# Performance work log

Measured on AMD Instinct MI355X. Metric: run time of the kernel, lower is better.

## Reference

```python
import jax, jax.numpy as jnp
import numpy as np

B, T_IN, T_OUT = 32, 256, 512
N_MEL, E = 80, 512
A_RNN, D_RNN, PRENET, A_DIM = 1024, 1024, 256, 128
N_FILT, KSIZE = 32, 31


def setup_inputs() -> dict:
    key = jax.random.key(0)
    ks = jax.random.split(key, 20)
    def w(k, shape):
        fan_in = shape[-1] if len(shape) == 2 else shape[1] * shape[2]
        return jax.random.normal(k, shape, jnp.float32) / np.sqrt(fan_in)
    return dict(
        memory=jax.random.normal(ks[0], (B, T_IN, E), jnp.float32),
        decoder_inputs=jax.random.normal(ks[1], (B, N_MEL, T_OUT), jnp.float32),
        memory_lengths=jax.random.randint(ks[2], (B,), T_IN // 2, T_IN + 1).astype(jnp.int32),
        prenet_w1=w(ks[3], (PRENET, N_MEL)),
        prenet_w2=w(ks[4], (PRENET, PRENET)),
        att_rnn_wih=w(ks[5], (4 * A_RNN, PRENET + E)),
        att_rnn_whh=w(ks[6], (4 * A_RNN, A_RNN)),
        att_rnn_b=jnp.zeros((4 * A_RNN,), jnp.float32),
        wq=w(ks[7], (A_DIM, A_RNN)),
        wm=w(ks[8], (A_DIM, E)),
        v=w(ks[9], (1, A_DIM)),
        loc_conv=w(ks[10], (N_FILT, 2, KSIZE)),
        loc_dense=w(ks[11], (A_DIM, N_FILT)),
        dec_rnn_wih=w(ks[12], (4 * D_RNN, A_RNN + E)),
        dec_rnn_whh=w(ks[13], (4 * D_RNN, D_RNN)),
        dec_rnn_b=jnp.zeros((4 * D_RNN,), jnp.float32),
        proj_w=w(ks[14], (N_MEL, D_RNN + E)),
        proj_b=jnp.zeros((N_MEL,), jnp.float32),
        gate_w=w(ks[15], (1, D_RNN + E)),
        gate_b=jnp.zeros((1,), jnp.float32),
    )


def _lstm_cell(x, h, c, wih, whh, b):
    g = x @ wih.T + h @ whh.T + b
    i, f, gg, o = jnp.split(g, 4, axis=-1)
    c2 = jax.nn.sigmoid(f) * c + jax.nn.sigmoid(i) * jnp.tanh(gg)
    h2 = jax.nn.sigmoid(o) * jnp.tanh(c2)
    return h2, c2


def reference(memory, decoder_inputs, memory_lengths, prenet_w1, prenet_w2,
              att_rnn_wih, att_rnn_whh, att_rnn_b, wq, wm, v, loc_conv, loc_dense,
              dec_rnn_wih, dec_rnn_whh, dec_rnn_b, proj_w, proj_b, gate_w, gate_b):
    Bc, Tin, Ec = memory.shape
    # True where padded (masked out of attention)
    pad_mask = jnp.arange(Tin)[None, :] >= memory_lengths[:, None]
    processed_memory = memory @ wm.T  # (B, T_in, A_DIM)

    # parse decoder inputs: (B, n_mel, T_out) -> (T_out, B, n_mel); prepend go frame
    dec_seq = jnp.transpose(decoder_inputs, (2, 0, 1))
    go = jnp.zeros((1, Bc, N_MEL), dec_seq.dtype)
    dec_seq = jnp.concatenate([go, dec_seq], axis=0)[:-1]  # teacher-forced inputs
    # prenet (eval; stochastic dropout removed for determinism)
    x = jax.nn.relu(dec_seq @ prenet_w1.T)
    x = jax.nn.relu(x @ prenet_w2.T)  # (T_out, B, PRENET)

    NEG = jnp.asarray(-1e9, memory.dtype)
    pad = KSIZE // 2

    def step(carry, xt):
        ah, ac, dh, dc, aw, awc, ctx = carry
        # attention RNN
        ah, ac = _lstm_cell(jnp.concatenate([xt, ctx], -1), ah, ac,
                            att_rnn_wih, att_rnn_whh, att_rnn_b)
        # location-sensitive attention
        cat = jnp.stack([aw, awc], axis=1)  # (B, 2, T_in)
        loc = jax.lax.conv_general_dilated(cat, loc_conv, (1,), [(pad, pad)],
                                           dimension_numbers=('NCH', 'OIH', 'NCH'))
        loc = jnp.transpose(loc, (0, 2, 1)) @ loc_dense.T  # (B, T_in, A_DIM)
        pq = ah @ wq.T  # (B, A_DIM)
        e = jnp.tanh(pq[:, None, :] + loc + processed_memory) @ v[0]  # (B, T_in)
        e = jnp.where(pad_mask, NEG, e)
        wgt = jax.nn.softmax(e, axis=1)
        ctx = jnp.einsum('bt,bte->be', wgt, memory)
        awc = awc + wgt
        # decoder RNN
        dh, dc = _lstm_cell(jnp.concatenate([ah, ctx], -1), dh, dc,
                            dec_rnn_wih, dec_rnn_whh, dec_rnn_b)
        pi = jnp.concatenate([dh, ctx], -1)
        mel = pi @ proj_w.T + proj_b
        gate = (pi @ gate_w.T + gate_b)[:, 0]
        return (ah, ac, dh, dc, wgt, awc, ctx), (mel, gate, wgt)

    z = lambda *s: jnp.zeros(s, memory.dtype)
    carry0 = (z(Bc, A_RNN), z(Bc, A_RNN), z(Bc, D_RNN), z(Bc, D_RNN),
              z(Bc, Tin), z(Bc, Tin), z(Bc, Ec))
    _, (mels, gates, aligns) = jax.lax.scan(step, carry0, x)
    mel_out = jnp.transpose(mels, (1, 2, 0))      # (B, n_mel, T_out)
    gate_out = gates.T                             # (B, T_out)
    align_out = jnp.transpose(aligns, (1, 0, 2))   # (B, T_out, T_in)
    return mel_out, gate_out, align_out
```

## Files before the change

### kernel.cpp

```cpp
#include <hip/hip_runtime.h>
#include <hip/hip_bf16.h>
#include <math.h>

typedef __attribute__((ext_vector_type(8))) short bf16x8;
typedef __attribute__((ext_vector_type(4))) float f32x4;

#define B_X2    0u
#define B_PM    8388608u
#define B_WSA   12582912u
#define B_WSD   27262976u
#define B_AHB0  48234496u
#define B_AHB1  48300032u
#define B_DHB0  48365568u
#define B_DHB1  48431104u
#define B_CTXB  48496640u
#define B_AC    48529408u
#define B_DC    48660480u
#define B_AWC   48791552u
#define B_ZERO_START 48234496u
#define B_ZERO_BYTES 589824u
#define B_AHF   48824320u
#define B_DHF0  48955392u
#define B_CTXF0 49086464u
#define B_CTXF1 49152000u
#define B_DHF1  49217536u
#define B_LPM   49348608u
#define B_WQT   53542912u

#define OUT_MEL   0u
#define OUT_GATE  1310720u
#define OUT_ALIGN 1327104u

#define QSM_BYTES 23040

__device__ __forceinline__ float sigf(float x) { return 1.f / (1.f + expf(-x)); }
__device__ __forceinline__ float ftanh(float x) {
    float t = exp2f(x * 2.885390081777927f);
    return 1.f - 2.f * __builtin_amdgcn_rcpf(t + 1.f);
}

#define HOLD(s, b0, b1) (((s) & 1) ? (b0) : (b1))

__global__ __launch_bounds__(256) void prenet_kernel(
    const float* __restrict__ dec_in,
    const float* __restrict__ w1,
    const float* __restrict__ w2,
    __hip_bfloat16* __restrict__ x2)
{
    int b  = blockIdx.x & 31;
    int t0 = (blockIdx.x >> 5) * 16;
    __shared__ float xin[16][80];
    __shared__ float h1[16][257];

    for (int i = threadIdx.x; i < 16 * 80; i += 256) {
        int tt = i / 80, m = i - tt * 80;
        int t = t0 + tt;
        xin[tt][m] = (t == 0) ? 0.f
                   : dec_in[(size_t)b * 80 * 512 + (size_t)m * 512 + (t - 1)];
    }
    __syncthreads();
    for (int i = threadIdx.x; i < 16 * 256; i += 256) {
        int tt = i >> 8, p = i & 255;
        const float* wr = w1 + p * 80;
        float s = 0.f;
        for (int m = 0; m < 80; ++m) s += xin[tt][m] * wr[m];
        h1[tt][p] = fmaxf(s, 0.f);
    }
    __syncthreads();
    for (int i = threadIdx.x; i < 16 * 256; i += 256) {
        int tt = i >> 8, q = i & 255;
        const float* wr = w2 + q * 256;
        float s = 0.f;
        for (int p = 0; p < 256; ++p) s += h1[tt][p] * wr[p];
        int t = t0 + tt;
        x2[(size_t)t * (32 * 256) + b * 256 + q] = __float2bfloat16(fmaxf(s, 0.f));
    }
}

__global__ __launch_bounds__(128) void pm_kernel(
    const float* __restrict__ memory,
    const float* __restrict__ wm,
    float* __restrict__ pm)
{
    int b = blockIdx.y, tt0 = blockIdx.x * 16;
    __shared__ float ms[16][513];
    for (int i = threadIdx.x; i < 16 * 512; i += 128) {
        int tt = i >> 9, e = i & 511;
        ms[tt][e] = memory[(size_t)b * 131072 + (size_t)(tt0 + tt) * 512 + e];
    }
    __syncthreads();
    int d = threadIdx.x;
    float acc[16];
#pragma unroll
    for (int i = 0; i < 16; ++i) acc[i] = 0.f;
    const float* wr = wm + d * 512;
    for (int e = 0; e < 512; ++e) {
        float w = wr[e];
#pragma unroll
        for (int ttl = 0; ttl < 16; ++ttl) acc[ttl] += w * ms[ttl][e];
    }
    for (int ttl = 0; ttl < 16; ++ttl)
        pm[(size_t)b * 32768 + (size_t)(tt0 + ttl) * 128 + d] = acc[ttl];
}

__global__ __launch_bounds__(256) void swizzle_kernel(
    const float* __restrict__ wih, int Kih,
    const float* __restrict__ whh, int Khh,
    __hip_bfloat16* __restrict__ out, int K)
{
    int idx = blockIdx.x * 256 + threadIdx.x;
    int lane = idx & 63;
    int tk = idx >> 6;
    int KB = K >> 5;
    int nt = tk / KB, kb = tk - nt * KB;
    int c = lane & 15;
    int n = (c >> 2) * 1024 + nt * 4 + (c & 3);
    int k = kb * 32 + ((lane >> 4) << 3);
    const float* src; int kk;
    if (k < Kih) { src = wih + (size_t)n * Kih; kk = k; }
    else         { src = whh + (size_t)n * Khh; kk = k - Kih; }
    __hip_bfloat16* op = out + (size_t)idx * 8;
#pragma unroll
    for (int j = 0; j < 8; ++j) op[j] = __float2bfloat16(src[kk + j]);
}

__global__ __launch_bounds__(256) void wqt_kernel(
    const float* __restrict__ wq,
    float* __restrict__ wqT)
{
    int idx = blockIdx.x * 256 + threadIdx.x;
    int k = idx >> 7, d = idx & 127;
    wqT[idx] = wq[(size_t)d * 1024 + k];
}

template<int K, int S0, int S1, int S0STR, int S1STR, int S2STR>
__device__ __forceinline__ void lstm_tile(
    char* smem, int nt,
    const __hip_bfloat16* __restrict__ seg0,
    const __hip_bfloat16* __restrict__ seg1,
    const __hip_bfloat16* __restrict__ seg2,
    const __hip_bfloat16* __restrict__ wsw,
    const float* __restrict__ bias,
    float* __restrict__ c_state,
    float* __restrict__ h_f32,
    __hip_bfloat16* __restrict__ h_bf16)
{
    constexpr int KB  = K / 32;
    constexpr int NCH = K / 256;

    float (*red)[2][4][64] = (float(*)[2][4][64])smem;
    float (*gsum)[17]      = (float(*)[17])(smem + 16384);

    int tid  = threadIdx.x;
    int lane = tid & 63;
    int w    = tid >> 6;
    int r0   = lane & 15;
    int kq   = (lane >> 4) << 3;

    const __hip_bfloat16* wp = wsw + (((size_t)nt * KB + (size_t)w * NCH) * 64 + lane) * 8;
    f32x4 acc0 = {0.f, 0.f, 0.f, 0.f};
    f32x4 acc1 = {0.f, 0.f, 0.f, 0.f};
    int k0 = w * (K / 8);

#pragma unroll
    for (int i = 0; i < NCH; ++i) {
        int kc = k0 + i * 32;
        const __hip_bfloat16* sp; int sstr, off;
        if (kc < S0)           { sp = seg0; sstr = S0STR; off = kc; }
        else if (kc < S0 + S1) { sp = seg1; sstr = S1STR; off = kc - S0; }
        else                   { sp = seg2; sstr = S2STR; off = kc - S0 - S1; }
        int ko = off + kq;
        bf16x8 a0 = *(const bf16x8*)(sp + (size_t)r0 * sstr + ko);
        bf16x8 a1 = *(const bf16x8*)(sp + (size_t)(r0 + 16) * sstr + ko);
        bf16x8 bb = *(const bf16x8*)(wp + (size_t)i * 512);
        acc0 = __builtin_amdgcn_mfma_f32_16x16x32_bf16(a0, bb, acc0, 0, 0, 0);
        acc1 = __builtin_amdgcn_mfma_f32_16x16x32_bf16(a1, bb, acc1, 0, 0, 0);
    }

#pragma unroll
    for (int r = 0; r < 4; ++r) {
        red[w][0][r][lane] = acc0[r];
        red[w][1][r][lane] = acc1[r];
    }
    __syncthreads();

    {
        int b = tid >> 4, c = tid & 15;
        int mt = b >> 4, bm = b & 15;
        int lidx = ((bm >> 2) << 4) + c, rg = bm & 3;
        float s = 0.f;
#pragma unroll
        for (int ks = 0; ks < 8; ++ks) s += red[ks][mt][rg][lidx];
        gsum[b][c] = s;
    }
    __syncthreads();

    if (tid < 128) {
        int b = tid & 31, jl = tid >> 5;
        int j = nt * 4 + jl;
        float gi = gsum[b][jl]      + bias[j];
        float gf = gsum[b][4 + jl]  + bias[1024 + j];
        float gg = gsum[b][8 + jl]  + bias[2048 + j];
        float go = gsum[b][12 + jl] + bias[3072 + j];
        float cv = c_state[b * 1024 + j];
        float c2 = sigf(gf) * cv + sigf(gi) * tanhf(gg);
        float h2 = sigf(go) * tanhf(c2);
        c_state[b * 1024 + j] = c2;
        h_f32[b * 1024 + j]   = h2;
        h_bf16[b * 1024 + j]  = __float2bfloat16(h2);
    }
}

__global__ __launch_bounds__(512, 2) void qstep_kernel(
    const __hip_bfloat16* __restrict__ x2b,
    __hip_bfloat16* __restrict__ ctxb,
    __hip_bfloat16* __restrict__ ahb0, __hip_bfloat16* __restrict__ ahb1,
    __hip_bfloat16* __restrict__ dhb0, __hip_bfloat16* __restrict__ dhb1,
    const __hip_bfloat16* __restrict__ wswA,
    const __hip_bfloat16* __restrict__ wswD,
    const float* __restrict__ a_b, const float* __restrict__ d_b,
    float* __restrict__ ac, float* __restrict__ dc,
    float* __restrict__ ahf,
    float* __restrict__ dhf0, float* __restrict__ dhf1,
    const float* __restrict__ ctxf0, const float* __restrict__ ctxf1,
    const float* __restrict__ proj_w, const float* __restrict__ proj_b,
    const float* __restrict__ gate_w, const float* __restrict__ gate_b,
    float* __restrict__ out_mel, float* __restrict__ out_gate,
    const float* __restrict__ lconv, const float* __restrict__ ldense,
    const float* __restrict__ pm,
    const float* __restrict__ awc, const float* __restrict__ align_out,
    float* __restrict__ lpmbuf,
    int t)
{
    __shared__ char smem[QSM_BYTES];
    int blk = blockIdx.x;
    int tid = threadIdx.x;

    if (blk < 256) {
        if (t < 0) return;
        lstm_tile<2560, 1024, 512, 1024, 512, 1024>(
            smem, blk,
            HOLD(t, ahb0, ahb1), ctxb, HOLD(t - 1, dhb0, dhb1),
            wswD, d_b, dc,
            HOLD(t, dhf1, dhf0), HOLD(t, dhb0, dhb1));
        return;
    }

    if (blk < 512) {
        int s = t + 1;
        if (s > 511) return;
        lstm_tile<1792, 256, 512, 256, 512, 1024>(
            smem, blk - 256,
            x2b + (size_t)s * 8192, ctxb, HOLD(s - 1, ahb0, ahb1),
            wswA, a_b, ac, ahf, HOLD(s, ahb0, ahb1));
        return;
    }

    if (blk < 544) {
        if (t + 1 > 511) return;
        int b = blk - 512;
        __hip_bfloat16 (*locb)[40] = (__hip_bfloat16(*)[40])smem;
        float* aw_s  = (float*)(smem + 20480);
        float* awc_s = (float*)(smem + 21632);

        if (tid < 288) {
            int tt = tid - 15;
            float a = 0.f, c = 0.f;
            if (tt >= 0 && tt < 256) {
                a = (t >= 0) ? align_out[(size_t)b * 131072 + (size_t)t * 256 + tt] : 0.f;
                c = awc[b * 256 + tt];
            }
            aw_s[tid] = a; awc_s[tid] = c;
        }
        __syncthreads();

        for (int it = 0; it < 2; ++it) {
            int item = tid + it * 512;
            int f = item >> 5, ttg = item & 31;
            const float* kcA = lconv + f * 62;
            const float* kcB = kcA + 31;
            float ka[31], kb_[31];
#pragma unroll
            for (int k = 0; k < 31; ++k) { ka[k] = kcA[k]; kb_[k] = kcB[k]; }
            float acc[8];
#pragma unroll
            for (int s = 0; s < 8; ++s) acc[s] = 0.f;
            int base = ttg * 8;
#pragma unroll
            for (int u = 0; u < 38; ++u) {
                float av = aw_s[base + u];
                float cv = awc_s[base + u];
#pragma unroll
                for (int s = 0; s < 8; ++s) {
                    int k = u - s;
                    if (k >= 0 && k < 31) {
                        acc[s] = fmaf(ka[k], av, acc[s]);
                        acc[s] = fmaf(kb_[k], cv, acc[s]);
                    }
                }
            }
#pragma unroll
            for (int s = 0; s < 8; ++s)
                locb[base + s][f] = __float2bfloat16(acc[s]);
        }
        __syncthreads();

        {
            int lane = tid & 63;
            int w    = tid >> 6;
            int c    = lane & 15, q = lane >> 4;

            bf16x8 Bf[8];
#pragma unroll
            for (int tc = 0; tc < 8; ++tc) {
                int d = tc * 16 + c;
                const float* lp = ldense + d * 32 + q * 8;
                float4 f0 = *(const float4*)lp;
                float4 f1 = *(const float4*)(lp + 4);
                union { bf16x8 vv; __hip_bfloat16 h[8]; } u;
                u.h[0] = __float2bfloat16(f0.x); u.h[1] = __float2bfloat16(f0.y);
                u.h[2] = __float2bfloat16(f0.z); u.h[3] = __float2bfloat16(f0.w);
                u.h[4] = __float2bfloat16(f1.x); u.h[5] = __float2bfloat16(f1.y);
                u.h[6] = __float2bfloat16(f1.z); u.h[7] = __float2bfloat16(f1.w);
                Bf[tc] = u.vv;
            }
#pragma unroll
            for (int half = 0; half < 2; ++half) {
                int mt = w * 2 + half;
                bf16x8 Af = *(const bf16x8*)&locb[mt * 16 + c][q * 8];
                f32x4 zero = {0.f, 0.f, 0.f, 0.f};
#pragma unroll
                for (int tc = 0; tc < 8; ++tc) {
                    f32x4 P = __builtin_amdgcn_mfma_f32_16x16x32_bf16(Af, Bf[tc], zero, 0, 0, 0);
                    int d = tc * 16 + c;
#pragma unroll
                    for (int r = 0; r < 4; ++r) {
                        int ttp = mt * 16 + q * 4 + r;
                        size_t ix = ((size_t)b << 15) + (size_t)ttp * 128 + d;
                        lpmbuf[ix] = P[r] + pm[ix];
                    }
                }
            }
        }
        return;
    }

    {
        if (t < 1) return;
        int pb = blk - 544;
        int b = pb >> 1, half = pb & 1;
        int tp = t - 1;
        const float* dh = HOLD(tp, dhf1, dhf0);
        const float* cx = HOLD(tp, ctxf1, ctxf0);
        float* pi = (float*)smem;
        for (int i = tid; i < 1024; i += 512) pi[i] = dh[b * 1024 + i];
        if (tid < 512) pi[1024 + tid] = cx[b * 512 + tid];
        __syncthreads();
        int w = tid >> 6, lane = tid & 63;
        int nOut = half ? 41 : 40;
        for (int o = w; o < nOut; o += 8) {
            bool isGate = (half && o == 40);
            int m = half * 40 + o;
            const float* wr = isGate ? gate_w : (proj_w + (size_t)m * 1536);
            float s = 0.f;
#pragma unroll
            for (int c = 0; c < 6; ++c) {
                float4 wv = *(const float4*)(wr + c * 256 + lane * 4);
                const float* pp = pi + c * 256 + lane * 4;
                s += wv.x * pp[0] + wv.y * pp[1] + wv.z * pp[2] + wv.w * pp[3];
            }
#pragma unroll
            for (int mm = 32; mm >= 1; mm >>= 1) s += __shfl_xor(s, mm);
            if (lane == 0) {
                if (isGate) out_gate[b * 512 + tp] = s + gate_b[0];
                else out_mel[(size_t)b * (80 * 512) + (size_t)m * 512 + tp]
                        = s + proj_b[m];
            }
        }
    }
}

__global__ __launch_bounds__(1024) void attn_kernel(
    const float* __restrict__ memory,
    const int*   __restrict__ mlen,
    const float* __restrict__ wqT,
    const float* __restrict__ v,
    const float* __restrict__ lpmbuf,
    const float* __restrict__ ahf,
    float* __restrict__ ctxf_cur,
    __hip_bfloat16* __restrict__ ctxb,
    float* __restrict__ awc,
    float* __restrict__ align_out,
    int t)
{
    int b = blockIdx.x, tid = threadIdx.x;
    __shared__ float red[1024];
    __shared__ float pq_s[128];
    __shared__ float v_s[128];
    __shared__ float wgt_s[256];

    int len = mlen[b];

    if (tid < 128) v_s[tid] = v[tid];
    {
        int p = tid >> 7, d = tid & 127;
        const float* wt = wqT + (size_t)(p * 128) * 128 + d;
        const float* hh = ahf + b * 1024 + p * 128;
        float s0 = 0.f, s1 = 0.f, s2 = 0.f, s3 = 0.f;
#pragma unroll 8
        for (int kk = 0; kk < 128; kk += 4) {
            s0 = fmaf(hh[kk],     wt[(size_t)kk * 128],       s0);
            s1 = fmaf(hh[kk + 1], wt[(size_t)(kk + 1) * 128], s1);
            s2 = fmaf(hh[kk + 2], wt[(size_t)(kk + 2) * 128], s2);
            s3 = fmaf(hh[kk + 3], wt[(size_t)(kk + 3) * 128], s3);
        }
        red[tid] = (s0 + s1) + (s2 + s3);
    }
    __syncthreads();

    if (tid < 128) {
        float s = 0.f;
#pragma unroll
        for (int p = 0; p < 8; ++p) s += red[p * 128 + tid];
        pq_s[tid] = s;
    }
    __syncthreads();

    {
        int ttc = tid >> 2, dg = tid & 3;
        const float4* lp4 = (const float4*)(lpmbuf + ((size_t)b << 15) + (size_t)ttc * 128 + dg * 32);
        const float4* pq4 = (const float4*)(pq_s + dg * 32);
        const float4* v4  = (const float4*)(v_s + dg * 32);
        float pe = 0.f;
#pragma unroll
        for (int j = 0; j < 8; ++j) {
            float4 x = lp4[j], pq = pq4[j], vv = v4[j];
            pe += ftanh(x.x + pq.x) * vv.x + ftanh(x.y + pq.y) * vv.y
                + ftanh(x.z + pq.z) * vv.z + ftanh(x.w + pq.w) * vv.w;
        }
        __syncthreads();
        red[tid] = pe;
    }
    __syncthreads();

    if (tid < 64) {
        float ev[4];
        float mx = -1e30f;
#pragma unroll
        for (int r = 0; r < 4; ++r) {
            int tt = tid * 4 + r;
            float e = red[tt * 4] + red[tt * 4 + 1] + red[tt * 4 + 2] + red[tt * 4 + 3];
            ev[r] = (tt < len) ? e : -1e9f;
            mx = fmaxf(mx, ev[r]);
        }
#pragma unroll
        for (int mm = 32; mm >= 1; mm >>= 1) mx = fmaxf(mx, __shfl_xor(mx, mm));
        float sum = 0.f;
#pragma unroll
        for (int r = 0; r < 4; ++r) {
            ev[r] = exp2f((ev[r] - mx) * 1.4426950408889634f);
            sum += ev[r];
        }
#pragma unroll
        for (int mm = 32; mm >= 1; mm >>= 1) sum += __shfl_xor(sum, mm);
        float winv = __builtin_amdgcn_rcpf(sum);
#pragma unroll
        for (int r = 0; r < 4; ++r) {
            int tt = tid * 4 + r;
            float wg = ev[r] * winv;
            wgt_s[tt] = wg;
            align_out[(size_t)b * 131072 + (size_t)t * 256 + tt] = wg;
            awc[b * 256 + tt] += wg;
        }
    }
    __syncthreads();

    {
        int ee = tid & 511, p = tid >> 9;
        const float* mr = memory + (size_t)b * 131072 + ee;
        float s0 = 0.f, s1 = 0.f, s2 = 0.f, s3 = 0.f;
        float s4 = 0.f, s5 = 0.f, s6 = 0.f, s7 = 0.f;
        int t0 = p * 128;
        for (int ttl = 0; ttl < 128; ttl += 8) {
            int tt = t0 + ttl;
            s0 = fmaf(wgt_s[tt],     mr[(size_t)tt * 512],       s0);
            s1 = fmaf(wgt_s[tt + 1], mr[(size_t)(tt + 1) * 512], s1);
            s2 = fmaf(wgt_s[tt + 2], mr[(size_t)(tt + 2) * 512], s2);
            s3 = fmaf(wgt_s[tt + 3], mr[(size_t)(tt + 3) * 512], s3);
            s4 = fmaf(wgt_s[tt + 4], mr[(size_t)(tt + 4) * 512], s4);
            s5 = fmaf(wgt_s[tt + 5], mr[(size_t)(tt + 5) * 512], s5);
            s6 = fmaf(wgt_s[tt + 6], mr[(size_t)(tt + 6) * 512], s6);
            s7 = fmaf(wgt_s[tt + 7], mr[(size_t)(tt + 7) * 512], s7);
        }
        red[p * 512 + ee] = ((s0 + s1) + (s2 + s3)) + ((s4 + s5) + (s6 + s7));
    }
    __syncthreads();
    if (tid < 512) {
        float cv = red[tid] + red[512 + tid];
        ctxf_cur[b * 512 + tid] = cv;
        ctxb[b * 512 + tid] = __float2bfloat16(cv);
    }
}

__global__ __launch_bounds__(256) void proj_kernel(
    const float* __restrict__ dh,
    const float* __restrict__ ctx,
    const float* __restrict__ proj_w,
    const float* __restrict__ proj_b,
    const float* __restrict__ gate_w,
    const float* __restrict__ gate_b,
    float* __restrict__ out_mel,
    float* __restrict__ out_gate,
    int t)
{
    int b = blockIdx.x, tid = threadIdx.x;
    __shared__ float pi[1536];
    __shared__ float red[256];
    for (int i = tid; i < 1024; i += 256) pi[i] = dh[b * 1024 + i];
    for (int i = tid; i < 512; i += 256) pi[1024 + i] = ctx[b * 512 + i];
    __syncthreads();

    float s = 0.f;
    if (tid < 240) {
        int m = tid / 3, p = tid - m * 3;
        const float* wr = proj_w + (size_t)m * 1536 + p * 512;
        const float* pr = pi + p * 512;
        for (int k = 0; k < 512; ++k) s += wr[k] * pr[k];
    } else {
        int p = tid - 240;
        const float* wr = gate_w + p * 96;
        const float* pr = pi + p * 96;
        for (int k = 0; k < 96; ++k) s += wr[k] * pr[k];
    }
    red[tid] = s;
    __syncthreads();
    if (tid < 80) {
        float m3 = red[tid * 3] + red[tid * 3 + 1] + red[tid * 3 + 2];
        out_mel[(size_t)b * (80 * 512) + (size_t)tid * 512 + t] = m3 + proj_b[tid];
    } else if (tid == 80) {
        float g = gate_b[0];
#pragma unroll
        for (int p = 0; p < 16; ++p) g += red[240 + p];
        out_gate[b * 512 + t] = g;
    }
}

extern "C" void kernel_launch(void* const* d_in, const int* in_sizes, int n_in,
                              void* d_out, int out_size, void* d_ws, size_t ws_size,
                              hipStream_t stream)
{
    const float* memory   = (const float*)d_in[0];
    const float* dec_in   = (const float*)d_in[1];
    const int*   mlen     = (const int*)  d_in[2];
    const float* pw1      = (const float*)d_in[3];
    const float* pw2      = (const float*)d_in[4];
    const float* a_wih    = (const float*)d_in[5];
    const float* a_whh    = (const float*)d_in[6];
    const float* a_b      = (const float*)d_in[7];
    const float* wq       = (const float*)d_in[8];
    const float* wm       = (const float*)d_in[9];
    const float* v        = (const float*)d_in[10];
    const float* lconv    = (const float*)d_in[11];
    const float* ldense   = (const float*)d_in[12];
    const float* d_wih    = (const float*)d_in[13];
    const float* d_whh    = (const float*)d_in[14];
    const float* d_b      = (const float*)d_in[15];
    const float* proj_w   = (const float*)d_in[16];
    const float* proj_b   = (const float*)d_in[17];
    const float* gate_w   = (const float*)d_in[18];
    const float* gate_b   = (const float*)d_in[19];

    char* ws = (char*)d_ws;
    __hip_bfloat16* x2b  = (__hip_bfloat16*)(ws + B_X2);
    float*          pm   = (float*)(ws + B_PM);
    __hip_bfloat16* wswA = (__hip_bfloat16*)(ws + B_WSA);
    __hip_bfloat16* wswD = (__hip_bfloat16*)(ws + B_WSD);
    __hip_bfloat16* ahb0 = (__hip_bfloat16*)(ws + B_AHB0);
    __hip_bfloat16* ahb1 = (__hip_bfloat16*)(ws + B_AHB1);
    __hip_bfloat16* dhb0 = (__hip_bfloat16*)(ws + B_DHB0);
    __hip_bfloat16* dhb1 = (__hip_bfloat16*)(ws + B_DHB1);
    __hip_bfloat16* ctxb = (__hip_bfloat16*)(ws + B_CTXB);
    float*          ac   = (float*)(ws + B_AC);
    float*          dc   = (float*)(ws + B_DC);
    float*          awcp = (float*)(ws + B_AWC);
    float*          ahf  = (float*)(ws + B_AHF);
    float*          dhf0 = (float*)(ws + B_DHF0);
    float*          dhf1 = (float*)(ws + B_DHF1);
    float*          ctxf0= (float*)(ws + B_CTXF0);
    float*          ctxf1= (float*)(ws + B_CTXF1);
    float*          lpmb = (float*)(ws + B_LPM);
    float*          wqt  = (float*)(ws + B_WQT);

    float* out       = (float*)d_out;
    float* out_mel   = out + OUT_MEL;
    float* out_gate  = out + OUT_GATE;
    float* out_align = out + OUT_ALIGN;

    hipMemsetAsync(ws + B_ZERO_START, 0, B_ZERO_BYTES, stream);

    prenet_kernel<<<1024, 256, 0, stream>>>(dec_in, pw1, pw2, x2b);
    pm_kernel<<<dim3(16, 32), 128, 0, stream>>>(memory, wm, pm);
    swizzle_kernel<<<3584, 256, 0, stream>>>(a_wih, 768,  a_whh, 1024, wswA, 1792);
    swizzle_kernel<<<5120, 256, 0, stream>>>(d_wih, 1536, d_whh, 1024, wswD, 2560);
    wqt_kernel<<<512, 256, 0, stream>>>(wq, wqt);

    qstep_kernel<<<608, 512, 0, stream>>>(
        x2b, ctxb, ahb0, ahb1, dhb0, dhb1, wswA, wswD, a_b, d_b,
        ac, dc, ahf, dhf0, dhf1, ctxf0, ctxf1,
        proj_w, proj_b, gate_w, gate_b, out_mel, out_gate,
        lconv, ldense, pm, awcp, out_align, lpmb, -1);

    for (int t = 0; t < 512; ++t) {
        float* ctxf_cur = (t & 1) ? ctxf1 : ctxf0;

        attn_kernel<<<32, 1024, 0, stream>>>(
            memory, mlen, wqt, v, lpmb, ahf,
            ctxf_cur, ctxb, awcp, out_align, t);

        qstep_kernel<<<608, 512, 0, stream>>>(
            x2b, ctxb, ahb0, ahb1, dhb0, dhb1, wswA, wswD, a_b, d_b,
            ac, dc, ahf, dhf0, dhf1, ctxf0, ctxf1,
            proj_w, proj_b, gate_w, gate_b, out_mel, out_gate,
            lconv, ldense, pm, awcp, out_align, lpmb, t);
    }

    proj_kernel<<<32, 256, 0, stream>>>(
        dhf1, ctxf1, proj_w, proj_b, gate_w, gate_b,
        out_mel, out_gate, 511);
}
```

Baseline: 24.89 ms.

## Move projection blocks into attention kernel and halve attention-LSTM block count

The mel/gate projection work for step t-1 moves out of the per-step LSTM kernel and into a new kernel that also holds the attention blocks. The projection runs as 64 extra blocks alongside the 32 attention blocks, with 1024 threads each. Each attention-LSTM block now processes two tiles serially, so the LSTM kernel grid drops from 608 to 416 blocks. The aim is to rebalance work across the two per-step launches and fill idle CUs during the attention phase. The cost is a longer serial path per attention-LSTM block, which may lengthen the LSTM kernel's critical path.

```diff
diff --git a/kernel.cpp b/kernel.cpp
--- a/kernel.cpp
+++ b/kernel.cpp
@@ -31,6 +31,8 @@
 #define OUT_GATE  1310720u
 #define OUT_ALIGN 1327104u
 
+#define PSM_BYTES 6144
+
 #define QSM_BYTES 23040
 
 __device__ __forceinline__ float sigf(float x) { return 1.f / (1.f + expf(-x)); }
@@ -211,6 +213,175 @@
     }
 }
 
+__global__ __launch_bounds__(1024) void pstep_kernel(
+    const float* __restrict__ memory,
+    const int*   __restrict__ mlen,
+    const float* __restrict__ wqT,
+    const float* __restrict__ v,
+    const float* __restrict__ lpmbuf,
+    const float* __restrict__ ahf,
+    float* __restrict__ ctxf0, float* __restrict__ ctxf1,
+    __hip_bfloat16* __restrict__ ctxb,
+    float* __restrict__ awc,
+    float* __restrict__ align_out,
+    const float* __restrict__ dhf0, const float* __restrict__ dhf1,
+    const float* __restrict__ proj_w, const float* __restrict__ proj_b,
+    const float* __restrict__ gate_w, const float* __restrict__ gate_b,
+    float* __restrict__ out_mel, float* __restrict__ out_gate,
+    int t)
+{
+    __shared__ char smem[PSM_BYTES];
+    int blk = blockIdx.x;
+    int tid = threadIdx.x;
+
+    if (blk < 32) {
+        int b = blk;
+        float* red   = (float*)smem;
+        float* pq_s  = (float*)(smem + 4096);
+        float* v_s   = (float*)(smem + 4608);
+        float* wgt_s = (float*)(smem + 5120);
+
+        int len = mlen[b];
+
+        if (tid < 128) v_s[tid] = v[tid];
+        {
+            int p = tid >> 7, d = tid & 127;
+            const float* wt = wqT + (size_t)(p * 128) * 128 + d;
+            const float* hh = ahf + b * 1024 + p * 128;
+            float s0 = 0.f, s1 = 0.f, s2 = 0.f, s3 = 0.f;
+#pragma unroll 8
+            for (int kk = 0; kk < 128; kk += 4) {
+                s0 = fmaf(hh[kk],     wt[(size_t)kk * 128],       s0);
+                s1 = fmaf(hh[kk + 1], wt[(size_t)(kk + 1) * 128], s1);
+                s2 = fmaf(hh[kk + 2], wt[(size_t)(kk + 2) * 128], s2);
+                s3 = fmaf(hh[kk + 3], wt[(size_t)(kk + 3) * 128], s3);
+            }
+            red[tid] = (s0 + s1) + (s2 + s3);
+        }
+        __syncthreads();
+
+        if (tid < 128) {
+            float s = 0.f;
+#pragma unroll
+            for (int p = 0; p < 8; ++p) s += red[p * 128 + tid];
+            pq_s[tid] = s;
+        }
+        __syncthreads();
+
+        {
+            int ttc = tid >> 2, dg = tid & 3;
+            const float4* lp4 = (const float4*)(lpmbuf + ((size_t)b << 15) + (size_t)ttc * 128 + dg * 32);
+            const float4* pq4 = (const float4*)(pq_s + dg * 32);
+            const float4* v4  = (const float4*)(v_s + dg * 32);
+            float pe = 0.f;
+#pragma unroll
+            for (int j = 0; j < 8; ++j) {
+                float4 x = lp4[j], pq = pq4[j], vv = v4[j];
+                pe += ftanh(x.x + pq.x) * vv.x + ftanh(x.y + pq.y) * vv.y
+                    + ftanh(x.z + pq.z) * vv.z + ftanh(x.w + pq.w) * vv.w;
+            }
+            __syncthreads();
+            red[tid] = pe;
+        }
+        __syncthreads();
+
+        if (tid < 64) {
+            float ev[4];
+            float mx = -1e30f;
+#pragma unroll
+            for (int r = 0; r < 4; ++r) {
+                int tt = tid * 4 + r;
+                float e = red[tt * 4] + red[tt * 4 + 1] + red[tt * 4 + 2] + red[tt * 4 + 3];
+                ev[r] = (tt < len) ? e : -1e9f;
+                mx = fmaxf(mx, ev[r]);
+            }
+#pragma unroll
+            for (int mm = 32; mm >= 1; mm >>= 1) mx = fmaxf(mx, __shfl_xor(mx, mm));
+            float sum = 0.f;
+#pragma unroll
+            for (int r = 0; r < 4; ++r) {
+                ev[r] = exp2f((ev[r] - mx) * 1.4426950408889634f);
+                sum += ev[r];
+            }
+#pragma unroll
+            for (int mm = 32; mm >= 1; mm >>= 1) sum += __shfl_xor(sum, mm);
+            float winv = __builtin_amdgcn_rcpf(sum);
+#pragma unroll
+            for (int r = 0; r < 4; ++r) {
+                int tt = tid * 4 + r;
+                float wg = ev[r] * winv;
+                wgt_s[tt] = wg;
+                align_out[(size_t)b * 131072 + (size_t)t * 256 + tt] = wg;
+                awc[b * 256 + tt] += wg;
+            }
+        }
+        __syncthreads();
+
+        {
+            int ee = tid & 511, p = tid >> 9;
+            const float* mr = memory + (size_t)b * 131072 + ee;
+            float s0 = 0.f, s1 = 0.f, s2 = 0.f, s3 = 0.f;
+            float s4 = 0.f, s5 = 0.f, s6 = 0.f, s7 = 0.f;
+            int t0 = p * 128;
+            for (int ttl = 0; ttl < 128; ttl += 8) {
+                int tt = t0 + ttl;
+                s0 = fmaf(wgt_s[tt],     mr[(size_t)tt * 512],       s0);
+                s1 = fmaf(wgt_s[tt + 1], mr[(size_t)(tt + 1) * 512], s1);
+                s2 = fmaf(wgt_s[tt + 2], mr[(size_t)(tt + 2) * 512], s2);
+                s3 = fmaf(wgt_s[tt + 3], mr[(size_t)(tt + 3) * 512], s3);
+                s4 = fmaf(wgt_s[tt + 4], mr[(size_t)(tt + 4) * 512], s4);
+                s5 = fmaf(wgt_s[tt + 5], mr[(size_t)(tt + 5) * 512], s5);
+                s6 = fmaf(wgt_s[tt + 6], mr[(size_t)(tt + 6) * 512], s6);
+                s7 = fmaf(wgt_s[tt + 7], mr[(size_t)(tt + 7) * 512], s7);
+            }
+            red[p * 512 + ee] = ((s0 + s1) + (s2 + s3)) + ((s4 + s5) + (s6 + s7));
+        }
+        __syncthreads();
+        if (tid < 512) {
+            float cv = red[tid] + red[512 + tid];
+            float* ctxf_cur = HOLD(t, ctxf1, ctxf0);
+            ctxf_cur[b * 512 + tid] = cv;
+            ctxb[b * 512 + tid] = __float2bfloat16(cv);
+        }
+        return;
+    }
+
+    {
+        if (t < 1) return;
+        int pb = blk - 32;
+        int b = pb >> 1, half = pb & 1;
+        int tp = t - 1;
+        const float* dh = HOLD(tp, dhf1, dhf0);
+        const float* cx = HOLD(tp, ctxf1, ctxf0);
+        float* pi = (float*)smem;
+        if (tid < 1024) pi[tid] = dh[b * 1024 + tid];
+        else ;
+        if (tid < 512) pi[1024 + tid] = cx[b * 512 + tid];
+        __syncthreads();
+        int w = tid >> 6, lane = tid & 63;
+        int nOut = half ? 41 : 40;
+        for (int o = w; o < nOut; o += 16) {
+            bool isGate = (half && o == 40);
+            int m = half * 40 + o;
+            const float* wr = isGate ? gate_w : (proj_w + (size_t)m * 1536);
+            float s = 0.f;
+#pragma unroll
+            for (int c = 0; c < 6; ++c) {
+                float4 wv = *(const float4*)(wr + c * 256 + lane * 4);
+                const float* pp = pi + c * 256 + lane * 4;
+                s += wv.x * pp[0] + wv.y * pp[1] + wv.z * pp[2] + wv.w * pp[3];
+            }
+#pragma unroll
+            for (int mm = 32; mm >= 1; mm >>= 1) s += __shfl_xor(s, mm);
+            if (lane == 0) {
+                if (isGate) out_gate[b * 512 + tp] = s + gate_b[0];
+                else out_mel[(size_t)b * (80 * 512) + (size_t)m * 512 + tp]
+                        = s + proj_b[m];
+            }
+        }
+    }
+}
+
 __global__ __launch_bounds__(512, 2) void qstep_kernel(
     const __hip_bfloat16* __restrict__ x2b,
     __hip_bfloat16* __restrict__ ctxb,
@@ -222,10 +393,6 @@
     float* __restrict__ ac, float* __restrict__ dc,
     float* __restrict__ ahf,
     float* __restrict__ dhf0, float* __restrict__ dhf1,
-    const float* __restrict__ ctxf0, const float* __restrict__ ctxf1,
-    const float* __restrict__ proj_w, const float* __restrict__ proj_b,
-    const float* __restrict__ gate_w, const float* __restrict__ gate_b,
-    float* __restrict__ out_mel, float* __restrict__ out_gate,
     const float* __restrict__ lconv, const float* __restrict__ ldense,
     const float* __restrict__ pm,
     const float* __restrict__ awc, const float* __restrict__ align_out,
@@ -246,19 +413,24 @@
         return;
     }
 
-    if (blk < 512) {
+    if (blk < 384) {
         int s = t + 1;
         if (s > 511) return;
-        lstm_tile<1792, 256, 512, 256, 512, 1024>(
-            smem, blk - 256,
-            x2b + (size_t)s * 8192, ctxb, HOLD(s - 1, ahb0, ahb1),
-            wswA, a_b, ac, ahf, HOLD(s, ahb0, ahb1));
+        int base = (blk - 256) * 2;
+#pragma unroll
+        for (int h = 0; h < 2; ++h) {
+            if (h) __syncthreads();
+            lstm_tile<1792, 256, 512, 256, 512, 1024>(
+                smem, base + h,
+                x2b + (size_t)s * 8192, ctxb, HOLD(s - 1, ahb0, ahb1),
+                wswA, a_b, ac, ahf, HOLD(s, ahb0, ahb1));
+        }
         return;
     }
 
-    if (blk < 544) {
+    {
         if (t + 1 > 511) return;
-        int b = blk - 512;
+        int b = blk - 384;
         __hip_bfloat16 (*locb)[40] = (__hip_bfloat16(*)[40])smem;
         float* aw_s  = (float*)(smem + 20480);
         float* awc_s = (float*)(smem + 21632);
@@ -342,163 +514,6 @@
                 }
             }
         }
-        return;
-    }
-
-    {
-        if (t < 1) return;
-        int pb = blk - 544;
-        int b = pb >> 1, half = pb & 1;
-        int tp = t - 1;
-        const float* dh = HOLD(tp, dhf1, dhf0);
-        const float* cx = HOLD(tp, ctxf1, ctxf0);
-        float* pi = (float*)smem;
-        for (int i = tid; i < 1024; i += 512) pi[i] = dh[b * 1024 + i];
-        if (tid < 512) pi[1024 + tid] = cx[b * 512 + tid];
-        __syncthreads();
-        int w = tid >> 6, lane = tid & 63;
-        int nOut = half ? 41 : 40;
-        for (int o = w; o < nOut; o += 8) {
-            bool isGate = (half && o == 40);
-            int m = half * 40 + o;
-            const float* wr = isGate ? gate_w : (proj_w + (size_t)m * 1536);
-            float s = 0.f;
-#pragma unroll
-            for (int c = 0; c < 6; ++c) {
-                float4 wv = *(const float4*)(wr + c * 256 + lane * 4);
-                const float* pp = pi + c * 256 + lane * 4;
-                s += wv.x * pp[0] + wv.y * pp[1] + wv.z * pp[2] + wv.w * pp[3];
-            }
-#pragma unroll
-            for (int mm = 32; mm >= 1; mm >>= 1) s += __shfl_xor(s, mm);
-            if (lane == 0) {
-                if (isGate) out_gate[b * 512 + tp] = s + gate_b[0];
-                else out_mel[(size_t)b * (80 * 512) + (size_t)m * 512 + tp]
-                        = s + proj_b[m];
-            }
-        }
-    }
-}
-
-__global__ __launch_bounds__(1024) void attn_kernel(
-    const float* __restrict__ memory,
-    const int*   __restrict__ mlen,
-    const float* __restrict__ wqT,
-    const float* __restrict__ v,
-    const float* __restrict__ lpmbuf,
-    const float* __restrict__ ahf,
-    float* __restrict__ ctxf_cur,
-    __hip_bfloat16* __restrict__ ctxb,
-    float* __restrict__ awc,
-    float* __restrict__ align_out,
-    int t)
-{
-    int b = blockIdx.x, tid = threadIdx.x;
-    __shared__ float red[1024];
-    __shared__ float pq_s[128];
-    __shared__ float v_s[128];
-    __shared__ float wgt_s[256];
-
-    int len = mlen[b];
-
-    if (tid < 128) v_s[tid] = v[tid];
-    {
-        int p = tid >> 7, d = tid & 127;
-        const float* wt = wqT + (size_t)(p * 128) * 128 + d;
-        const float* hh = ahf + b * 1024 + p * 128;
-        float s0 = 0.f, s1 = 0.f, s2 = 0.f, s3 = 0.f;
-#pragma unroll 8
-        for (int kk = 0; kk < 128; kk += 4) {
-            s0 = fmaf(hh[kk],     wt[(size_t)kk * 128],       s0);
-            s1 = fmaf(hh[kk + 1], wt[(size_t)(kk + 1) * 128], s1);
-            s2 = fmaf(hh[kk + 2], wt[(size_t)(kk + 2) * 128], s2);
-            s3 = fmaf(hh[kk + 3], wt[(size_t)(kk + 3) * 128], s3);
-        }
-        red[tid] = (s0 + s1) + (s2 + s3);
-    }
-    __syncthreads();
-
-    if (tid < 128) {
-        float s = 0.f;
-#pragma unroll
-        for (int p = 0; p < 8; ++p) s += red[p * 128 + tid];
-        pq_s[tid] = s;
-    }
-    __syncthreads();
-
-    {
-        int ttc = tid >> 2, dg = tid & 3;
-        const float4* lp4 = (const float4*)(lpmbuf + ((size_t)b << 15) + (size_t)ttc * 128 + dg * 32);
-        const float4* pq4 = (const float4*)(pq_s + dg * 32);
-        const float4* v4  = (const float4*)(v_s + dg * 32);
-        float pe = 0.f;
-#pragma unroll
-        for (int j = 0; j < 8; ++j) {
-            float4 x = lp4[j], pq = pq4[j], vv = v4[j];
-            pe += ftanh(x.x + pq.x) * vv.x + ftanh(x.y + pq.y) * vv.y
-                + ftanh(x.z + pq.z) * vv.z + ftanh(x.w + pq.w) * vv.w;
-        }
-        __syncthreads();
-        red[tid] = pe;
-    }
-    __syncthreads();
-
-    if (tid < 64) {
-        float ev[4];
-        float mx = -1e30f;
-#pragma unroll
-        for (int r = 0; r < 4; ++r) {
-            int tt = tid * 4 + r;
-            float e = red[tt * 4] + red[tt * 4 + 1] + red[tt * 4 + 2] + red[tt * 4 + 3];
-            ev[r] = (tt < len) ? e : -1e9f;
-            mx = fmaxf(mx, ev[r]);
-        }
-#pragma unroll
-        for (int mm = 32; mm >= 1; mm >>= 1) mx = fmaxf(mx, __shfl_xor(mx, mm));
-        float sum = 0.f;
-#pragma unroll
-        for (int r = 0; r < 4; ++r) {
-            ev[r] = exp2f((ev[r] - mx) * 1.4426950408889634f);
-            sum += ev[r];
-        }
-#pragma unroll
-        for (int mm = 32; mm >= 1; mm >>= 1) sum += __shfl_xor(sum, mm);
-        float winv = __builtin_amdgcn_rcpf(sum);
-#pragma unroll
-        for (int r = 0; r < 4; ++r) {
-            int tt = tid * 4 + r;
-            float wg = ev[r] * winv;
-            wgt_s[tt] = wg;
-            align_out[(size_t)b * 131072 + (size_t)t * 256 + tt] = wg;
-            awc[b * 256 + tt] += wg;
-        }
-    }
-    __syncthreads();
-
-    {
-        int ee = tid & 511, p = tid >> 9;
-        const float* mr = memory + (size_t)b * 131072 + ee;
-        float s0 = 0.f, s1 = 0.f, s2 = 0.f, s3 = 0.f;
-        float s4 = 0.f, s5 = 0.f, s6 = 0.f, s7 = 0.f;
-        int t0 = p * 128;
-        for (int ttl = 0; ttl < 128; ttl += 8) {
-            int tt = t0 + ttl;
-            s0 = fmaf(wgt_s[tt],     mr[(size_t)tt * 512],       s0);
-            s1 = fmaf(wgt_s[tt + 1], mr[(size_t)(tt + 1) * 512], s1);
-            s2 = fmaf(wgt_s[tt + 2], mr[(size_t)(tt + 2) * 512], s2);
-            s3 = fmaf(wgt_s[tt + 3], mr[(size_t)(tt + 3) * 512], s3);
-            s4 = fmaf(wgt_s[tt + 4], mr[(size_t)(tt + 4) * 512], s4);
-            s5 = fmaf(wgt_s[tt + 5], mr[(size_t)(tt + 5) * 512], s5);
-            s6 = fmaf(wgt_s[tt + 6], mr[(size_t)(tt + 6) * 512], s6);
-            s7 = fmaf(wgt_s[tt + 7], mr[(size_t)(tt + 7) * 512], s7);
-        }
-        red[p * 512 + ee] = ((s0 + s1) + (s2 + s3)) + ((s4 + s5) + (s6 + s7));
-    }
-    __syncthreads();
-    if (tid < 512) {
-        float cv = red[tid] + red[512 + tid];
-        ctxf_cur[b * 512 + tid] = cv;
-        ctxb[b * 512 + tid] = __float2bfloat16(cv);
     }
 }
 
@@ -604,23 +619,21 @@
     swizzle_kernel<<<5120, 256, 0, stream>>>(d_wih, 1536, d_whh, 1024, wswD, 2560);
     wqt_kernel<<<512, 256, 0, stream>>>(wq, wqt);
 
-    qstep_kernel<<<608, 512, 0, stream>>>(
+    qstep_kernel<<<416, 512, 0, stream>>>(
         x2b, ctxb, ahb0, ahb1, dhb0, dhb1, wswA, wswD, a_b, d_b,
-        ac, dc, ahf, dhf0, dhf1, ctxf0, ctxf1,
-        proj_w, proj_b, gate_w, gate_b, out_mel, out_gate,
+        ac, dc, ahf, dhf0, dhf1,
         lconv, ldense, pm, awcp, out_align, lpmb, -1);
 
     for (int t = 0; t < 512; ++t) {
-        float* ctxf_cur = (t & 1) ? ctxf1 : ctxf0;
-
-        attn_kernel<<<32, 1024, 0, stream>>>(
+        pstep_kernel<<<96, 1024, 0, stream>>>(
             memory, mlen, wqt, v, lpmb, ahf,
-            ctxf_cur, ctxb, awcp, out_align, t);
-
-        qstep_kernel<<<608, 512, 0, stream>>>(
+            ctxf0, ctxf1, ctxb, awcp, out_align,
+            dhf0, dhf1,
+            proj_w, proj_b, gate_w, gate_b, out_mel, out_gate, t);
+
+        qstep_kernel<<<416, 512, 0, stream>>>(
             x2b, ctxb, ahb0, ahb1, dhb0, dhb1, wswA, wswD, a_b, d_b,
-            ac, dc, ahf, dhf0, dhf1, ctxf0, ctxf1,
-            proj_w, proj_b, gate_w, gate_b, out_mel, out_gate,
+            ac, dc, ahf, dhf0, dhf1,
             lconv, ldense, pm, awcp, out_align, lpmb, t);
     }
 
```

New measurement: 22.76 ms. -8.6%, faster.
